# Kernel optimization log

Measured on AMD Instinct MI355X. Metric: run time of the kernel, lower is better.

The kernel has to match this reference:

```python
import jax, jax.numpy as jnp
import numpy as np

N = 8192        # total nodes in the batch of graphs
E = 262144      # edges (avg degree 32)
F_IN = 128      # input node features
G = 64          # graphs in batch
C = 10          # classes
K1, K2, K3 = 4096, 2048, 1024  # int(0.5*N), int(0.5*K1), int(0.5*K2)


def setup_inputs() -> dict:
    key = jax.random.key(0)
    ks = jax.random.split(key, 16)
    def lin(k, i, o):
        return jax.random.normal(k, (i, o), jnp.float32) / np.float32(np.sqrt(i))
    return {
        "x": jax.random.normal(ks[0], (N, F_IN), jnp.float32),
        "edge_index": jax.random.randint(ks[1], (2, E), 0, N),
        "batch": jnp.sort(jax.random.randint(ks[2], (N,), 0, G)),
        "W1": lin(ks[3], F_IN, 32), "b1": jnp.zeros((32,), jnp.float32),
        "W2": lin(ks[4], 32, 64),   "b2": jnp.zeros((64,), jnp.float32),
        "W3": lin(ks[5], 64, 128),  "b3": jnp.zeros((128,), jnp.float32),
        "W4": lin(ks[6], 128, 256), "b4": jnp.zeros((256,), jnp.float32),
        "W5": lin(ks[7], 384, 128), "b5": jnp.zeros((128,), jnp.float32),
        "W6": lin(ks[8], 192, 64),  "b6": jnp.zeros((64,), jnp.float32),
        "W7": lin(ks[9], 96, 32),   "b7": jnp.zeros((32,), jnp.float32),
        "p1": jax.random.normal(ks[10], (32,), jnp.float32),
        "p2": jax.random.normal(ks[11], (64,), jnp.float32),
        "p3": jax.random.normal(ks[12], (128,), jnp.float32),
        "Wl1": lin(ks[13], 64, 64),
        "Wc": lin(ks[14], 64, C), "bc": jnp.zeros((C,), jnp.float32),
    }


def _gcn(A, x, W, b):
    # PyG GCNConv (improved=False): out = D^-1/2 (A+I) D^-1/2 propagated src->dst.
    n = A.shape[0]
    Ah = A + jnp.eye(n, dtype=A.dtype)
    deg = Ah.sum(axis=0)                                  # degree at targets (cols)
    dinv = jnp.where(deg > 0, deg ** -0.5, 0.0).astype(A.dtype)
    An = dinv[:, None] * Ah * dinv[None, :]               # edge norm d[src]^-.5 * d[dst]^-.5
    return An.T @ (x @ W) + b                             # out[dst] += norm * (xW)[src]


def _gpool(A, x, p, k):
    # GPool: scores = Linear(x)/||p||, top-k select, gate by sigmoid, reindex dense adj.
    scores = (x @ p) / jnp.linalg.norm(p)                 # [n]
    vals, idx = jax.lax.top_k(scores, k)
    xp = x[idx] * jax.nn.sigmoid(vals)[:, None]
    Ap = (A[idx][:, idx] > 0).astype(x.dtype)             # dense_to_sparse rebinarizes
    return xp, Ap, idx


def reference(x, edge_index, batch, W1, b1, W2, b2, W3, b3, W4, b4, W5, b5,
              W6, b6, W7, b7, p1, p2, p3, Wl1, Wc, bc):
    elu = jax.nn.elu
    # to_dense_adj: dense N x N adjacency (duplicate edges accumulate)
    A = jnp.zeros((N, N), x.dtype).at[edge_index[0], edge_index[1]].add(1.0)
    x1 = elu(_gcn(A, x, W1, b1))
    x2, A2, i2 = _gpool(A, x1, p1, K1); x2 = elu(x2)
    x3 = elu(_gcn(A2, x2, W2, b2))
    x4, A4, i4 = _gpool(A2, x3, p2, K2); x4 = elu(x4)
    x5 = elu(_gcn(A4, x4, W3, b3))
    x6, A6, i6 = _gpool(A4, x5, p3, K3); x6 = elu(x6)
    x7 = elu(_gcn(A6, x6, W4, b4))
    u = jnp.zeros((K2, x7.shape[1]), x7.dtype).at[i6].set(x7)   # GUnpool
    x8 = elu(jnp.concatenate([u, x5], axis=1))
    x9 = elu(_gcn(A4, x8, W5, b5))
    u = jnp.zeros((K1, x9.shape[1]), x9.dtype).at[i4].set(x9)
    x10 = elu(jnp.concatenate([u, x3], axis=1))
    x11 = elu(_gcn(A2, x10, W6, b6))
    u = jnp.zeros((N, x11.shape[1]), x11.dtype).at[i2].set(x11)
    x12 = elu(jnp.concatenate([u, x1], axis=1))
    x13 = elu(_gcn(A, x12, W7, b7))
    gmax = jax.ops.segment_max(x13, batch, num_segments=G)      # global max pool
    gsum = jax.ops.segment_sum(x13, batch, num_segments=G)
    cnt = jax.ops.segment_sum(jnp.ones((N, 1), x13.dtype), batch, num_segments=G)
    h = elu(jnp.concatenate([gmax, gsum / cnt], axis=1))        # [G, 64]
    h = elu(h @ Wl1)
    return jax.nn.log_softmax(h @ Wc + bc, axis=-1)
```

## Files before the change

### kernel.cpp

```cpp
#include <hip/hip_runtime.h>
#include <math.h>

#define NN 8192
#define EE 262144
#define GG 64
#define CC 10
#define KK1 4096
#define KK2 2048
#define KK3 1024
#define PITCH 128

typedef unsigned long long ull;

__device__ __forceinline__ float eluf(float x) { return x > 0.f ? x : expm1f(x); }
__device__ __forceinline__ float sigf(float x) { return 1.f / (1.f + expf(-x)); }
__device__ __forceinline__ unsigned f2s(float f) {
    unsigned u = __float_as_uint(f);
    return (u & 0x80000000u) ? ~u : (u | 0x80000000u);
}

__global__ void k_init(const int* __restrict__ ei, unsigned* __restrict__ bitmap,
                       int* __restrict__ cnt1, int* __restrict__ csr1,
                       const int* __restrict__ batch, int* __restrict__ gstart,
                       const float* __restrict__ X, const float* __restrict__ W,
                       float* __restrict__ Y) {
    __shared__ float Xs[32][33];
    __shared__ float Ws[32][36];
    int tid = threadIdx.x;
    if ((int)blockIdx.x >= 1024) {
        int txn = tid & 7, tym = tid >> 3;
        int m0 = ((int)blockIdx.x - 1024) * 32;
        float4 acc = make_float4(0.f, 0.f, 0.f, 0.f);
        for (int k0 = 0; k0 < 128; k0 += 32) {
            int r = tid >> 3, c4 = (tid & 7) << 2;
            *(float4*)&Xs[r][c4] = *(const float4*)&X[(size_t)(m0 + r) * 128 + k0 + c4];
            *(float4*)&Ws[r][c4] = *(const float4*)&W[(size_t)(k0 + r) * 32 + c4];
            __syncthreads();
#pragma unroll 8
            for (int kk = 0; kk < 32; kk++) {
                float4 wv = *(const float4*)&Ws[kk][txn * 4];
                float xv = Xs[tym][kk];
                acc.x += xv * wv.x; acc.y += xv * wv.y;
                acc.z += xv * wv.z; acc.w += xv * wv.w;
            }
            __syncthreads();
        }
        *(float4*)&Y[(size_t)(m0 + tym) * 32 + txn * 4] = acc;
        return;
    }
    int e = blockIdx.x * 256 + tid;
    int s = ei[e], d = ei[EE + e];
    unsigned key = ((unsigned)s << 13) | (unsigned)d;
    unsigned old = atomicOr(&bitmap[key >> 5], 1u << (key & 31u));
    int dup = (old >> (key & 31u)) & 1;
    int pos = atomicAdd(&cnt1[d], 1);
    csr1[(d << 7) + pos] = dup ? (s | 0x80000000) : s;
    if (e < NN) {
        int g = batch[e];
        int prev = (e == 0) ? -1 : batch[e - 1];
        for (int gg = prev + 1; gg <= g; gg++) gstart[gg] = e;
        if (e == NN - 1)
            for (int gg = g + 1; gg <= GG; gg++) gstart[gg] = NN;
    }
}

template<int L1>
__global__ void k_pool_sub(const float* __restrict__ x, const float* __restrict__ score,
                           const int* __restrict__ idx, int k, int F,
                           float* __restrict__ xout, int nPool,
                           const int* __restrict__ csrP, const int* __restrict__ roffP,
                           const int* __restrict__ degP,
                           const int* __restrict__ invmap,
                           int* __restrict__ csrO, int* __restrict__ roffO,
                           int* __restrict__ degO, float* __restrict__ dinvO) {
    if ((int)blockIdx.x < nPool) {
        int t = blockIdx.x * 256 + threadIdx.x;
        if (t >= k * F) return;
        int r = t / F, f = t - r * F;
        int j = idx[r];
        xout[t] = eluf(x[(size_t)j * F + f] * sigf(score[j]));
        return;
    }
    int wid = (((int)blockIdx.x - nPool) * 256 + (int)threadIdx.x) >> 6;
    int lane = threadIdx.x & 63;
    if (wid >= k) return;
    int j = idx[wid];
    int j0 = L1 ? (j << 7) : roffP[j];
    int len = degP[j];
    int cnt = 0;
    for (int base = 0; base < len; base += 64) {
        bool sel = false;
        int val = 0;
        if (base + lane < len) {
            int e = csrP[j0 + base + lane];
            if (!L1 || e >= 0) {
                int s = L1 ? (e & 0x7fffffff) : e;
                int v = invmap[s];
                if (v > 0) { sel = true; val = v - 1; }
            }
        }
        ull m = __ballot(sel);
        if (sel) {
            int off = __popcll(m & ((1ull << lane) - 1ull));
            csrO[j0 + cnt + off] = val;
        }
        cnt += __popcll(m);
    }
    if (lane == 0) {
        roffO[wid] = j0;
        degO[wid] = cnt;
        dinvO[wid] = 1.f / sqrtf((float)(cnt + 1));
    }
}

__global__ void k_gemm(const float* __restrict__ X, const float* __restrict__ W,
                       float* __restrict__ Y, int M, int K, int F) {
    __shared__ float Xs[32][33];
    __shared__ float Ws[32][36];
    int tid = threadIdx.x;
    int txn = tid & 7, tym = tid >> 3;
    int m0 = blockIdx.x * 32, n0 = blockIdx.y * 32;
    float4 acc = make_float4(0.f, 0.f, 0.f, 0.f);
    for (int k0 = 0; k0 < K; k0 += 32) {
        {
            int r = tid >> 3, c4 = (tid & 7) << 2;
            *(float4*)&Xs[r][c4] = *(const float4*)&X[(size_t)(m0 + r) * K + k0 + c4];
            *(float4*)&Ws[r][c4] = *(const float4*)&W[(size_t)(k0 + r) * F + n0 + c4];
        }
        __syncthreads();
#pragma unroll 8
        for (int kk = 0; kk < 32; kk++) {
            float4 wv = *(const float4*)&Ws[kk][txn * 4];
            float xv = Xs[tym][kk];
            acc.x += xv * wv.x; acc.y += xv * wv.y;
            acc.z += xv * wv.z; acc.w += xv * wv.w;
        }
        __syncthreads();
    }
    *(float4*)&Y[(size_t)(m0 + tym) * F + n0 + txn * 4] = acc;
}

__global__ void k_gemm_up(const float* __restrict__ xl, const int* __restrict__ inv,
                          const float* __restrict__ xr, int Fl, int Fr,
                          const float* __restrict__ W, float* __restrict__ Y,
                          int M, int K, int F) {
    __shared__ float Xs[32][33];
    __shared__ float Ws[32][36];
    __shared__ int sIdx[32];
    int tid = threadIdx.x;
    int txn = tid & 7, tym = tid >> 3;
    int m0 = blockIdx.x * 32, n0 = blockIdx.y * 32;
    if (tid < 32) sIdx[tid] = inv[m0 + tid];
    float4 acc = make_float4(0.f, 0.f, 0.f, 0.f);
    __syncthreads();
    for (int k0 = 0; k0 < K; k0 += 32) {
        {
            int r = tid >> 3, c4 = (tid & 7) << 2;
            int kk = k0 + c4;
            float4 v;
            if (kk < Fl) {
                int rr = sIdx[r];
                v = (rr > 0) ? *(const float4*)&xl[(size_t)(rr - 1) * Fl + kk]
                             : make_float4(0.f, 0.f, 0.f, 0.f);
            } else {
                v = *(const float4*)&xr[(size_t)(m0 + r) * Fr + (kk - Fl)];
            }
            v.x = eluf(v.x); v.y = eluf(v.y); v.z = eluf(v.z); v.w = eluf(v.w);
            *(float4*)&Xs[r][c4] = v;
            *(float4*)&Ws[r][c4] = *(const float4*)&W[(size_t)(k0 + r) * F + n0 + c4];
        }
        __syncthreads();
#pragma unroll 8
        for (int kk = 0; kk < 32; kk++) {
            float4 wv = *(const float4*)&Ws[kk][txn * 4];
            float xv = Xs[tym][kk];
            acc.x += xv * wv.x; acc.y += xv * wv.y;
            acc.z += xv * wv.z; acc.w += xv * wv.w;
        }
        __syncthreads();
    }
    *(float4*)&Y[(size_t)(m0 + tym) * F + n0 + txn * 4] = acc;
}

template<int LOGF, int SCORE, int L1, int LS>
__global__ void k_prop(const int* __restrict__ csr, const int* __restrict__ roff,
                       const int* __restrict__ deg, const float* __restrict__ dinv,
                       const float* __restrict__ xW, const float* __restrict__ b,
                       float* __restrict__ xout, const float* __restrict__ p,
                       float* __restrict__ score) {
    constexpr int FQ = 1 << (LOGF - 2);
    constexpr int S = 1 << LS;
    constexpr int RL = FQ * S;
    const float4* xW4 = (const float4*)xW;
    int t = blockIdx.x * 256 + threadIdx.x;
    int d = t >> (LOGF - 2 + LS);
    int rem = t & (RL - 1);
    int q = rem >> LS, h = rem & (S - 1);
    int j0 = L1 ? (d << 7) : roff[d];
    int dg = deg[d];
    int j1 = j0 + dg;
    float dd = L1 ? (1.f / sqrtf((float)(dg + 1))) : dinv[d];
    int idx = (d << (LOGF - 2)) + q;
    float4 sum;
    if (h == 0) {
        float4 v0 = xW4[idx];
        sum = make_float4(dd * v0.x, dd * v0.y, dd * v0.z, dd * v0.w);
    } else {
        sum = make_float4(0.f, 0.f, 0.f, 0.f);
    }
    for (int j = j0 + h; j < j1; j += S) {
        int e = csr[j];
        int s = L1 ? (e & 0x7fffffff) : e;
        float ds = L1 ? (1.f / sqrtf((float)(deg[s] + 1))) : dinv[s];
        float4 xv = xW4[(s << (LOGF - 2)) + q];
        sum.x += ds * xv.x; sum.y += ds * xv.y;
        sum.z += ds * xv.z; sum.w += ds * xv.w;
    }
#pragma unroll
    for (int m = 1; m < S; m <<= 1) {
        sum.x += __shfl_xor(sum.x, m, 64);
        sum.y += __shfl_xor(sum.y, m, 64);
        sum.z += __shfl_xor(sum.z, m, 64);
        sum.w += __shfl_xor(sum.w, m, 64);
    }
    float4 bv = *(const float4*)&b[q << 2];
    float4 o;
    o.x = eluf(dd * sum.x + bv.x);
    o.y = eluf(dd * sum.y + bv.y);
    o.z = eluf(dd * sum.z + bv.z);
    o.w = eluf(dd * sum.w + bv.w);
    if (h == 0) ((float4*)xout)[idx] = o;
    if (SCORE) {
        float4 pv = *(const float4*)&p[q << 2];
        float sc = 0.f, nr = 0.f;
        if (h == 0) {
            sc = o.x * pv.x + o.y * pv.y + o.z * pv.z + o.w * pv.w;
            nr = pv.x * pv.x + pv.y * pv.y + pv.z * pv.z + pv.w * pv.w;
        }
#pragma unroll
        for (int m = RL >> 1; m >= 1; m >>= 1) {
            sc += __shfl_xor(sc, m, 64);
            nr += __shfl_xor(nr, m, 64);
        }
        if (rem == 0) score[d] = sc / sqrtf(nr);
    }
}

__device__ __forceinline__ ull cex_shfl(ull v, int st, bool takeMax) {
    ull pv = __shfl_xor(v, st, 64);
    return takeMax ? (v > pv ? v : pv) : (v < pv ? v : pv);
}
__device__ __forceinline__ void cexr(ull& a, ull& b, bool desc) {
    if (desc ? (a < b) : (a > b)) { ull x = a; a = b; b = x; }
}

__global__ void k_wsort(const float* __restrict__ score, ull* __restrict__ keys,
                        int last, int k, int* __restrict__ out_idx,
                        int* __restrict__ invmap) {
    __shared__ ull sk[2048];
    int tid = threadIdx.x;
    int base = blockIdx.x << 11;
    int giA = base + tid, giB = giA + 1024;
    ull a = ((ull)f2s(score[giA]) << 32) | (unsigned)(~giA);
    ull b = ((ull)f2s(score[giB]) << 32) | (unsigned)(~giB);
    for (int sz = 2; sz <= 2048; sz <<= 1) {
        int st = sz >> 1;
        if (st >= 64) {
            sk[tid] = a; sk[tid + 1024] = b;
            __syncthreads();
            for (; st >= 64; st >>= 1) {
                int i = ((tid & ~(st - 1)) << 1) | (tid & (st - 1));
                int j = i | st;
                ull u = sk[i], v = sk[j];
                bool desc = (((base + i) & sz) == 0);
                if (desc ? (u < v) : (u > v)) { sk[i] = v; sk[j] = u; }
                __syncthreads();
            }
            a = sk[tid]; b = sk[tid + 1024];
        }
        for (; st >= 1; st >>= 1) {
            bool low = (tid & st) == 0;
            bool descA = ((giA & sz) == 0);
            bool descB = ((giB & sz) == 0);
            a = cex_shfl(a, st, descA == low);
            b = cex_shfl(b, st, descB == low);
        }
    }
    if (last) {
        if (giA < k) {
            int j = (int)(~(unsigned)(a & 0xFFFFFFFFu));
            out_idx[giA] = j; invmap[j] = giA + 1;
        }
        if (giB < k) {
            int j = (int)(~(unsigned)(b & 0xFFFFFFFFu));
            out_idx[giB] = j; invmap[j] = giB + 1;
        }
    } else {
        keys[giA] = a; keys[giB] = b;
    }
}

__global__ void k_stage4k_m(ull* __restrict__ keys) {
    __shared__ ull sk[4096];
    int tid = threadIdx.x;
    int base = blockIdx.x << 12;
    bool desc = ((base & 4096) == 0);
    ull k0 = keys[base + tid], k1 = keys[base + tid + 1024];
    ull k2 = keys[base + tid + 2048], k3 = keys[base + tid + 3072];
    cexr(k0, k2, desc); cexr(k1, k3, desc);
    sk[tid] = k0; sk[tid + 1024] = k1; sk[tid + 2048] = k2; sk[tid + 3072] = k3;
    __syncthreads();
    for (int st = 1024; st >= 64; st >>= 1) {
        for (int pp = tid; pp < 2048; pp += 1024) {
            int i = ((pp & ~(st - 1)) << 1) | (pp & (st - 1));
            int j = i | st;
            ull u = sk[i], v = sk[j];
            if (desc ? (u < v) : (u > v)) { sk[i] = v; sk[j] = u; }
        }
        __syncthreads();
    }
    k0 = sk[tid]; k1 = sk[tid + 1024]; k2 = sk[tid + 2048]; k3 = sk[tid + 3072];
    for (int st = 32; st >= 1; st >>= 1) {
        bool low = (tid & st) == 0;
        k0 = cex_shfl(k0, st, desc == low);
        k1 = cex_shfl(k1, st, desc == low);
        k2 = cex_shfl(k2, st, desc == low);
        k3 = cex_shfl(k3, st, desc == low);
    }
    keys[base + tid] = k0; keys[base + tid + 1024] = k1;
    keys[base + tid + 2048] = k2; keys[base + tid + 3072] = k3;
}

__global__ void k_stage8k_f(const ull* __restrict__ keys, int* __restrict__ out_idx,
                            int* __restrict__ invmap) {
    __shared__ ull sk[4096];
    int tid = threadIdx.x;
    ull a0 = keys[tid],        a1 = keys[tid + 1024];
    ull a2 = keys[tid + 2048], a3 = keys[tid + 3072];
    ull b0 = keys[tid + 4096], b1 = keys[tid + 5120];
    ull b2 = keys[tid + 6144], b3 = keys[tid + 7168];
    cexr(a0, b0, true); cexr(a1, b1, true);
    cexr(a2, b2, true); cexr(a3, b3, true);
    cexr(a0, a2, true); cexr(a1, a3, true);
    sk[tid] = a0; sk[tid + 1024] = a1; sk[tid + 2048] = a2; sk[tid + 3072] = a3;
    __syncthreads();
    for (int st = 1024; st >= 64; st >>= 1) {
        for (int pp = tid; pp < 2048; pp += 1024) {
            int i = ((pp & ~(st - 1)) << 1) | (pp & (st - 1));
            int j = i | st;
            ull u = sk[i], v = sk[j];
            if (u < v) { sk[i] = v; sk[j] = u; }
        }
        __syncthreads();
    }
    a0 = sk[tid]; a1 = sk[tid + 1024]; a2 = sk[tid + 2048]; a3 = sk[tid + 3072];
    for (int st = 32; st >= 1; st >>= 1) {
        bool low = (tid & st) == 0;
        a0 = cex_shfl(a0, st, low);
        a1 = cex_shfl(a1, st, low);
        a2 = cex_shfl(a2, st, low);
        a3 = cex_shfl(a3, st, low);
    }
    int p, j;
    p = tid;        j = (int)(~(unsigned)(a0 & 0xFFFFFFFFu)); out_idx[p] = j; invmap[j] = p + 1;
    p = tid + 1024; j = (int)(~(unsigned)(a1 & 0xFFFFFFFFu)); out_idx[p] = j; invmap[j] = p + 1;
    p = tid + 2048; j = (int)(~(unsigned)(a2 & 0xFFFFFFFFu)); out_idx[p] = j; invmap[j] = p + 1;
    p = tid + 3072; j = (int)(~(unsigned)(a3 & 0xFFFFFFFFu)); out_idx[p] = j; invmap[j] = p + 1;
}

__global__ void k_stage4k_f(const ull* __restrict__ keys, int* __restrict__ out_idx,
                            int* __restrict__ invmap) {
    __shared__ ull sk[2048];
    int tid = threadIdx.x;
    ull a0 = keys[tid],        a1 = keys[tid + 1024];
    ull a2 = keys[tid + 2048], a3 = keys[tid + 3072];
    cexr(a0, a2, true); cexr(a1, a3, true);
    sk[tid] = a0; sk[tid + 1024] = a1;
    __syncthreads();
    for (int st = 1024; st >= 64; st >>= 1) {
        int i = ((tid & ~(st - 1)) << 1) | (tid & (st - 1));
        int j = i | st;
        ull u = sk[i], v = sk[j];
        if (u < v) { sk[i] = v; sk[j] = u; }
        __syncthreads();
    }
    a0 = sk[tid]; a1 = sk[tid + 1024];
    for (int st = 32; st >= 1; st >>= 1) {
        bool low = (tid & st) == 0;
        a0 = cex_shfl(a0, st, low);
        a1 = cex_shfl(a1, st, low);
    }
    int p, j;
    p = tid;        j = (int)(~(unsigned)(a0 & 0xFFFFFFFFu)); out_idx[p] = j; invmap[j] = p + 1;
    p = tid + 1024; j = (int)(~(unsigned)(a1 & 0xFFFFFFFFu)); out_idx[p] = j; invmap[j] = p + 1;
}

__global__ void k_seg2(const float* __restrict__ x13, const int* __restrict__ gstart,
                       float* __restrict__ gmaxf, float* __restrict__ gsum,
                       int* __restrict__ gcnt) {
    __shared__ float sm[8][32], ss[8][32];
    int g = blockIdx.x;
    int j0 = gstart[g], j1 = gstart[g + 1];
    int t = threadIdx.x;
    int f = t & 31, r = t >> 5;
    float m = -INFINITY, s = 0.f;
    for (int j = j0 + r; j < j1; j += 8) {
        float v = x13[(j << 5) + f];
        m = fmaxf(m, v);
        s += v;
    }
    sm[r][f] = m; ss[r][f] = s;
    __syncthreads();
    if (t < 32) {
        float mm = sm[0][t], sss = ss[0][t];
        for (int i = 1; i < 8; i++) { mm = fmaxf(mm, sm[i][t]); sss += ss[i][t]; }
        gmaxf[(g << 5) + t] = mm;
        gsum[(g << 5) + t] = sss;
        if (t == 0) gcnt[g] = j1 - j0;
    }
}

__global__ void k_head(const float* __restrict__ gmaxf, const float* __restrict__ gsum,
                       const int* __restrict__ gcnt, const float* __restrict__ Wl1,
                       const float* __restrict__ Wc, const float* __restrict__ bc,
                       float* __restrict__ out) {
    __shared__ float h0[GG * 64];
    __shared__ float h1[GG * 64];
    __shared__ float lg[GG * CC];
    int tid = threadIdx.x;
    for (int t = tid; t < GG * 64; t += blockDim.x) {
        int g = t >> 6, c = t & 63;
        float v;
        if (c < 32) v = gmaxf[(g << 5) + c];
        else v = gsum[(g << 5) + (c - 32)] / (float)gcnt[g];
        h0[t] = eluf(v);
    }
    __syncthreads();
    for (int t = tid; t < GG * 64; t += blockDim.x) {
        int g = t >> 6, j = t & 63;
        float s = 0.f;
        for (int k = 0; k < 64; k++) s += h0[(g << 6) + k] * Wl1[k * 64 + j];
        h1[t] = eluf(s);
    }
    __syncthreads();
    for (int t = tid; t < GG * CC; t += blockDim.x) {
        int g = t / CC, c = t - g * CC;
        float s = bc[c];
        for (int k = 0; k < 64; k++) s += h1[(g << 6) + k] * Wc[k * CC + c];
        lg[t] = s;
    }
    __syncthreads();
    if (tid < GG) {
        int g = tid;
        float m = -1e30f;
        for (int c = 0; c < CC; c++) m = fmaxf(m, lg[g * CC + c]);
        float se = 0.f;
        for (int c = 0; c < CC; c++) se += expf(lg[g * CC + c] - m);
        float lse = m + logf(se);
        for (int c = 0; c < CC; c++) out[g * CC + c] = lg[g * CC + c] - lse;
    }
}

static void run_topk(const float* score, ull* keys, int n, int k, int* out_idx,
                     int* invmap, hipStream_t stream) {
    if (n == 2048) {
        k_wsort<<<1, 1024, 0, stream>>>(score, keys, 1, k, out_idx, invmap);
    } else if (n == 4096) {
        k_wsort<<<2, 1024, 0, stream>>>(score, keys, 0, k, out_idx, invmap);
        k_stage4k_f<<<1, 1024, 0, stream>>>(keys, out_idx, invmap);
    } else {
        k_wsort<<<4, 1024, 0, stream>>>(score, keys, 0, k, out_idx, invmap);
        k_stage4k_m<<<2, 1024, 0, stream>>>(keys);
        k_stage8k_f<<<1, 1024, 0, stream>>>(keys, out_idx, invmap);
    }
}

extern "C" void kernel_launch(void* const* d_in, const int* in_sizes, int n_in,
                              void* d_out, int out_size, void* d_ws, size_t ws_size,
                              hipStream_t stream) {
    const float* x = (const float*)d_in[0];
    const int* ei = (const int*)d_in[1];
    const int* batch = (const int*)d_in[2];
    const float* W1 = (const float*)d_in[3];  const float* b1 = (const float*)d_in[4];
    const float* W2 = (const float*)d_in[5];  const float* b2 = (const float*)d_in[6];
    const float* W3 = (const float*)d_in[7];  const float* b3 = (const float*)d_in[8];
    const float* W4 = (const float*)d_in[9];  const float* b4 = (const float*)d_in[10];
    const float* W5 = (const float*)d_in[11]; const float* b5 = (const float*)d_in[12];
    const float* W6 = (const float*)d_in[13]; const float* b6 = (const float*)d_in[14];
    const float* W7 = (const float*)d_in[15]; const float* b7 = (const float*)d_in[16];
    const float* p1 = (const float*)d_in[17];
    const float* p2 = (const float*)d_in[18];
    const float* p3 = (const float*)d_in[19];
    const float* Wl1 = (const float*)d_in[20];
    const float* Wc = (const float*)d_in[21];
    const float* bc = (const float*)d_in[22];
    float* out = (float*)d_out;
    (void)in_sizes; (void)n_in; (void)out_size; (void)ws_size;

    char* w = (char*)d_ws;
    size_t off = 0;
    auto alloc = [&](size_t bytes) -> char* {
        char* p = w + off;
        off = (off + bytes + 255) & ~(size_t)255;
        return p;
    };

    size_t zero_begin = off;
    unsigned* bitmap = (unsigned*)alloc((size_t)NN * NN / 8);
    int* cnt1 = (int*)alloc(NN * 4);
    int* pos2 = (int*)alloc(NN * 4);
    int* inv4 = (int*)alloc(KK1 * 4);
    int* inv6 = (int*)alloc(KK2 * 4);
    size_t zero_len = off - zero_begin;

    float* dinv2 = (float*)alloc(KK1 * 4);
    float* dinv3 = (float*)alloc(KK2 * 4);
    float* dinv4 = (float*)alloc(KK3 * 4);
    int* roff2 = (int*)alloc(KK1 * 4); int* deg2 = (int*)alloc(KK1 * 4);
    int* roff3 = (int*)alloc(KK2 * 4); int* deg3 = (int*)alloc(KK2 * 4);
    int* roff4 = (int*)alloc(KK3 * 4); int* deg4 = (int*)alloc(KK3 * 4);
    int* csr1 = (int*)alloc((size_t)NN * PITCH * 4);
    int* csr2 = (int*)alloc((size_t)NN * PITCH * 4);
    int* csr3 = (int*)alloc((size_t)NN * PITCH * 4);
    int* csr4 = (int*)alloc((size_t)NN * PITCH * 4);
    float* xW = (float*)alloc((size_t)262144 * 4);
    float* x1 = (float*)alloc((size_t)NN * 32 * 4);
    float* x2 = (float*)alloc((size_t)KK1 * 32 * 4);
    float* x3 = (float*)alloc((size_t)KK1 * 64 * 4);
    float* x4 = (float*)alloc((size_t)KK2 * 64 * 4);
    float* x5 = (float*)alloc((size_t)KK2 * 128 * 4);
    float* x6 = (float*)alloc((size_t)KK3 * 128 * 4);
    float* x7 = (float*)alloc((size_t)KK3 * 256 * 4);
    float* x9 = (float*)alloc((size_t)KK2 * 128 * 4);
    float* x11 = (float*)alloc((size_t)KK1 * 64 * 4);
    float* x13 = (float*)alloc((size_t)NN * 32 * 4);
    float* score1 = (float*)alloc(NN * 4);
    float* score2 = (float*)alloc(KK1 * 4);
    float* score3 = (float*)alloc(KK2 * 4);
    int* i2 = (int*)alloc(KK1 * 4);
    int* i4 = (int*)alloc(KK2 * 4);
    int* i6 = (int*)alloc(KK3 * 4);
    ull* keys = (ull*)alloc((size_t)NN * 8);
    int* gstart = (int*)alloc((GG + 1) * 4);
    float* gmaxf = (float*)alloc(GG * 32 * 4);
    float* gsum = (float*)alloc(GG * 32 * 4);
    int* gcnt = (int*)alloc(GG * 4);

    hipMemsetAsync(w + zero_begin, 0, zero_len, stream);

    const int B = 256;
    k_init<<<1280, B, 0, stream>>>(ei, bitmap, cnt1, csr1, batch, gstart, x, W1, xW);

    k_prop<5, 1, 1, 3><<<2048, B, 0, stream>>>(csr1, nullptr, cnt1, nullptr, xW, b1,
                                               x1, p1, score1);

    run_topk(score1, keys, NN, KK1, i2, pos2, stream);
    k_pool_sub<1><<<512 + KK1 / 4, B, 0, stream>>>(x1, score1, i2, KK1, 32, x2, 512,
                                                   csr1, nullptr, cnt1, pos2,
                                                   csr2, roff2, deg2, dinv2);

    k_gemm<<<dim3(KK1 / 32, 2), B, 0, stream>>>(x2, W2, xW, KK1, 32, 64);
    k_prop<6, 1, 0, 2><<<1024, B, 0, stream>>>(csr2, roff2, deg2, dinv2, xW, b2,
                                               x3, p2, score2);

    run_topk(score2, keys, KK1, KK2, i4, inv4, stream);
    k_pool_sub<0><<<512 + KK2 / 4, B, 0, stream>>>(x3, score2, i4, KK2, 64, x4, 512,
                                                   csr2, roff2, deg2, inv4,
                                                   csr3, roff3, deg3, dinv3);

    k_gemm<<<dim3(KK2 / 32, 4), B, 0, stream>>>(x4, W3, xW, KK2, 64, 128);
    k_prop<7, 1, 0, 1><<<512, B, 0, stream>>>(csr3, roff3, deg3, dinv3, xW, b3,
                                              x5, p3, score3);

    run_topk(score3, keys, KK2, KK3, i6, inv6, stream);
    k_pool_sub<0><<<512 + KK3 / 4, B, 0, stream>>>(x5, score3, i6, KK3, 128, x6, 512,
                                                   csr3, roff3, deg3, inv6,
                                                   csr4, roff4, deg4, dinv4);

    k_gemm<<<dim3(KK3 / 32, 8), B, 0, stream>>>(x6, W4, xW, KK3, 128, 256);
    k_prop<8, 0, 0, 1><<<512, B, 0, stream>>>(csr4, roff4, deg4, dinv4, xW, b4,
                                              x7, nullptr, nullptr);

    k_gemm_up<<<dim3(KK2 / 32, 4), B, 0, stream>>>(x7, inv6, x5, 256, 128,
                                                   W5, xW, KK2, 384, 128);
    k_prop<7, 0, 0, 2><<<1024, B, 0, stream>>>(csr3, roff3, deg3, dinv3, xW, b5,
                                               x9, nullptr, nullptr);

    k_gemm_up<<<dim3(KK1 / 32, 2), B, 0, stream>>>(x9, inv4, x3, 128, 64,
                                                   W6, xW, KK1, 192, 64);
    k_prop<6, 0, 0, 2><<<1024, B, 0, stream>>>(csr2, roff2, deg2, dinv2, xW, b6,
                                               x11, nullptr, nullptr);

    k_gemm_up<<<dim3(NN / 32, 1), B, 0, stream>>>(x11, pos2, x1, 64, 32,
                                                  W7, xW, NN, 96, 32);
    k_prop<5, 0, 1, 3><<<2048, B, 0, stream>>>(csr1, nullptr, cnt1, nullptr, xW, b7,
                                               x13, nullptr, nullptr);

    k_seg2<<<GG, B, 0, stream>>>(x13, gstart, gmaxf, gsum, gcnt);
    k_head<<<1, 1024, 0, stream>>>(gmaxf, gsum, gcnt, Wl1, Wc, bc, out);
}
```

Before: 333.4 us.

## Replace bitmap edge dedup with warp-level dedup and fuse sort and head kernels

Drops the N×N/8-byte duplicate-edge bitmap. That removes its large memset and the random atomicOr traffic in k_init. Duplicate neighbours are now found inside the level-1 pool subgraph kernel by shuffle-comparing each row's up to 128 entries within a warp. The 4096-element top-k sort now runs as one full bitonic sort kernel (k_sort4k) instead of wsort plus a merge stage, and segment pooling is fused with the MLP head into one per-graph kernel. This saves launches and memory traffic, at the cost of an O(degree) serial shuffle loop per selected node and redundant per-block head computation.

```diff
diff --git a/kernel.cpp b/kernel.cpp
--- a/kernel.cpp
+++ b/kernel.cpp
@@ -19,11 +19,10 @@
     return (u & 0x80000000u) ? ~u : (u | 0x80000000u);
 }
 
-__global__ void k_init(const int* __restrict__ ei, unsigned* __restrict__ bitmap,
-                       int* __restrict__ cnt1, int* __restrict__ csr1,
-                       const int* __restrict__ batch, int* __restrict__ gstart,
-                       const float* __restrict__ X, const float* __restrict__ W,
-                       float* __restrict__ Y) {
+__global__ void k_init(const int* __restrict__ ei, int* __restrict__ cnt1,
+                       int* __restrict__ csr1, const int* __restrict__ batch,
+                       int* __restrict__ gstart, const float* __restrict__ X,
+                       const float* __restrict__ W, float* __restrict__ Y) {
     __shared__ float Xs[32][33];
     __shared__ float Ws[32][36];
     int tid = threadIdx.x;
@@ -50,11 +49,8 @@
     }
     int e = blockIdx.x * 256 + tid;
     int s = ei[e], d = ei[EE + e];
-    unsigned key = ((unsigned)s << 13) | (unsigned)d;
-    unsigned old = atomicOr(&bitmap[key >> 5], 1u << (key & 31u));
-    int dup = (old >> (key & 31u)) & 1;
     int pos = atomicAdd(&cnt1[d], 1);
-    csr1[(d << 7) + pos] = dup ? (s | 0x80000000) : s;
+    csr1[(d << 7) + pos] = s;
     if (e < NN) {
         int g = batch[e];
         int prev = (e == 0) ? -1 : batch[e - 1];
@@ -85,31 +81,59 @@
     int lane = threadIdx.x & 63;
     if (wid >= k) return;
     int j = idx[wid];
-    int j0 = L1 ? (j << 7) : roffP[j];
-    int len = degP[j];
     int cnt = 0;
-    for (int base = 0; base < len; base += 64) {
-        bool sel = false;
-        int val = 0;
-        if (base + lane < len) {
-            int e = csrP[j0 + base + lane];
-            if (!L1 || e >= 0) {
-                int s = L1 ? (e & 0x7fffffff) : e;
-                int v = invmap[s];
+    if (L1) {
+        int j0 = j << 7;
+        int len = degP[j];
+        int e0 = (lane < len) ? csrP[j0 + lane] : -1;
+        int e1 = (64 + lane < len) ? csrP[j0 + 64 + lane] : -1;
+        bool dup0 = false, dup1 = false;
+        for (int q = 0; q < len - 1; q++) {
+            int vq = (q < 64) ? __shfl(e0, q, 64) : __shfl(e1, q - 64, 64);
+            if (lane > q && e0 == vq) dup0 = true;
+            if (64 + lane > q && e1 == vq) dup1 = true;
+        }
+        {
+            bool sel = (lane < len) && !dup0;
+            int val = 0;
+            if (sel) { int v = invmap[e0]; if (v > 0) val = v - 1; else sel = false; }
+            ull m = __ballot(sel);
+            if (sel) { int off = __popcll(m & ((1ull << lane) - 1ull)); csrO[j0 + cnt + off] = val; }
+            cnt += __popcll(m);
+        }
+        {
+            bool sel = (64 + lane < len) && !dup1;
+            int val = 0;
+            if (sel) { int v = invmap[e1]; if (v > 0) val = v - 1; else sel = false; }
+            ull m = __ballot(sel);
+            if (sel) { int off = __popcll(m & ((1ull << lane) - 1ull)); csrO[j0 + cnt + off] = val; }
+            cnt += __popcll(m);
+        }
+        if (lane == 0) {
+            roffO[wid] = j0;
+            degO[wid] = cnt;
+            dinvO[wid] = 1.f / sqrtf((float)(cnt + 1));
+        }
+    } else {
+        int j0 = roffP[j];
+        int len = degP[j];
+        for (int base = 0; base < len; base += 64) {
+            bool sel = false;
+            int val = 0;
+            if (base + lane < len) {
+                int e = csrP[j0 + base + lane];
+                int v = invmap[e];
                 if (v > 0) { sel = true; val = v - 1; }
             }
-        }
-        ull m = __ballot(sel);
-        if (sel) {
-            int off = __popcll(m & ((1ull << lane) - 1ull));
-            csrO[j0 + cnt + off] = val;
-        }
-        cnt += __popcll(m);
-    }
-    if (lane == 0) {
-        roffO[wid] = j0;
-        degO[wid] = cnt;
-        dinvO[wid] = 1.f / sqrtf((float)(cnt + 1));
+            ull m = __ballot(sel);
+            if (sel) { int off = __popcll(m & ((1ull << lane) - 1ull)); csrO[j0 + cnt + off] = val; }
+            cnt += __popcll(m);
+        }
+        if (lane == 0) {
+            roffO[wid] = j0;
+            degO[wid] = cnt;
+            dinvO[wid] = 1.f / sqrtf((float)(cnt + 1));
+        }
     }
 }
 
@@ -209,8 +233,7 @@
         sum = make_float4(0.f, 0.f, 0.f, 0.f);
     }
     for (int j = j0 + h; j < j1; j += S) {
-        int e = csr[j];
-        int s = L1 ? (e & 0x7fffffff) : e;
+        int s = csr[j];
         float ds = L1 ? (1.f / sqrtf((float)(deg[s] + 1))) : dinv[s];
         float4 xv = xW4[(s << (LOGF - 2)) + q];
         sum.x += ds * xv.x; sum.y += ds * xv.y;
@@ -300,35 +323,51 @@
     }
 }
 
-__global__ void k_stage4k_m(ull* __restrict__ keys) {
+__global__ void k_sort4k(const float* __restrict__ score, ull* __restrict__ keys,
+                         int last, int k, int* __restrict__ out_idx,
+                         int* __restrict__ invmap) {
     __shared__ ull sk[4096];
     int tid = threadIdx.x;
     int base = blockIdx.x << 12;
-    bool desc = ((base & 4096) == 0);
-    ull k0 = keys[base + tid], k1 = keys[base + tid + 1024];
-    ull k2 = keys[base + tid + 2048], k3 = keys[base + tid + 3072];
-    cexr(k0, k2, desc); cexr(k1, k3, desc);
-    sk[tid] = k0; sk[tid + 1024] = k1; sk[tid + 2048] = k2; sk[tid + 3072] = k3;
-    __syncthreads();
-    for (int st = 1024; st >= 64; st >>= 1) {
-        for (int pp = tid; pp < 2048; pp += 1024) {
-            int i = ((pp & ~(st - 1)) << 1) | (pp & (st - 1));
-            int j = i | st;
-            ull u = sk[i], v = sk[j];
-            if (desc ? (u < v) : (u > v)) { sk[i] = v; sk[j] = u; }
-        }
-        __syncthreads();
-    }
-    k0 = sk[tid]; k1 = sk[tid + 1024]; k2 = sk[tid + 2048]; k3 = sk[tid + 3072];
-    for (int st = 32; st >= 1; st >>= 1) {
-        bool low = (tid & st) == 0;
-        k0 = cex_shfl(k0, st, desc == low);
-        k1 = cex_shfl(k1, st, desc == low);
-        k2 = cex_shfl(k2, st, desc == low);
-        k3 = cex_shfl(k3, st, desc == low);
-    }
-    keys[base + tid] = k0; keys[base + tid + 1024] = k1;
-    keys[base + tid + 2048] = k2; keys[base + tid + 3072] = k3;
+    int p0 = base + tid, p1 = p0 + 1024, p2 = p0 + 2048, p3 = p0 + 3072;
+    ull k0 = ((ull)f2s(score[p0]) << 32) | (unsigned)(~p0);
+    ull k1 = ((ull)f2s(score[p1]) << 32) | (unsigned)(~p1);
+    ull k2 = ((ull)f2s(score[p2]) << 32) | (unsigned)(~p2);
+    ull k3 = ((ull)f2s(score[p3]) << 32) | (unsigned)(~p3);
+    for (int sz = 2; sz <= 4096; sz <<= 1) {
+        int st = sz >> 1;
+        if (st >= 64) {
+            sk[tid] = k0; sk[tid + 1024] = k1; sk[tid + 2048] = k2; sk[tid + 3072] = k3;
+            __syncthreads();
+            for (; st >= 64; st >>= 1) {
+                for (int pp = tid; pp < 2048; pp += 1024) {
+                    int i = ((pp & ~(st - 1)) << 1) | (pp & (st - 1));
+                    int jj = i | st;
+                    ull u = sk[i], v = sk[jj];
+                    bool desc = (((base + i) & sz) == 0);
+                    if (desc ? (u < v) : (u > v)) { sk[i] = v; sk[jj] = u; }
+                }
+                __syncthreads();
+            }
+            k0 = sk[tid]; k1 = sk[tid + 1024]; k2 = sk[tid + 2048]; k3 = sk[tid + 3072];
+        }
+        for (; st >= 1; st >>= 1) {
+            bool low = (tid & st) == 0;
+            k0 = cex_shfl(k0, st, ((p0 & sz) == 0) == low);
+            k1 = cex_shfl(k1, st, ((p1 & sz) == 0) == low);
+            k2 = cex_shfl(k2, st, ((p2 & sz) == 0) == low);
+            k3 = cex_shfl(k3, st, ((p3 & sz) == 0) == low);
+        }
+    }
+    if (last) {
+        int j;
+        if (p0 < k) { j = (int)(~(unsigned)(k0 & 0xFFFFFFFFu)); out_idx[p0] = j; invmap[j] = p0 + 1; }
+        if (p1 < k) { j = (int)(~(unsigned)(k1 & 0xFFFFFFFFu)); out_idx[p1] = j; invmap[j] = p1 + 1; }
+        if (p2 < k) { j = (int)(~(unsigned)(k2 & 0xFFFFFFFFu)); out_idx[p2] = j; invmap[j] = p2 + 1; }
+        if (p3 < k) { j = (int)(~(unsigned)(k3 & 0xFFFFFFFFu)); out_idx[p3] = j; invmap[j] = p3 + 1; }
+    } else {
+        keys[p0] = k0; keys[p1] = k1; keys[p2] = k2; keys[p3] = k3;
+    }
 }
 
 __global__ void k_stage8k_f(const ull* __restrict__ keys, int* __restrict__ out_idx,
@@ -368,37 +407,11 @@
     p = tid + 3072; j = (int)(~(unsigned)(a3 & 0xFFFFFFFFu)); out_idx[p] = j; invmap[j] = p + 1;
 }
 
-__global__ void k_stage4k_f(const ull* __restrict__ keys, int* __restrict__ out_idx,
-                            int* __restrict__ invmap) {
-    __shared__ ull sk[2048];
-    int tid = threadIdx.x;
-    ull a0 = keys[tid],        a1 = keys[tid + 1024];
-    ull a2 = keys[tid + 2048], a3 = keys[tid + 3072];
-    cexr(a0, a2, true); cexr(a1, a3, true);
-    sk[tid] = a0; sk[tid + 1024] = a1;
-    __syncthreads();
-    for (int st = 1024; st >= 64; st >>= 1) {
-        int i = ((tid & ~(st - 1)) << 1) | (tid & (st - 1));
-        int j = i | st;
-        ull u = sk[i], v = sk[j];
-        if (u < v) { sk[i] = v; sk[j] = u; }
-        __syncthreads();
-    }
-    a0 = sk[tid]; a1 = sk[tid + 1024];
-    for (int st = 32; st >= 1; st >>= 1) {
-        bool low = (tid & st) == 0;
-        a0 = cex_shfl(a0, st, low);
-        a1 = cex_shfl(a1, st, low);
-    }
-    int p, j;
-    p = tid;        j = (int)(~(unsigned)(a0 & 0xFFFFFFFFu)); out_idx[p] = j; invmap[j] = p + 1;
-    p = tid + 1024; j = (int)(~(unsigned)(a1 & 0xFFFFFFFFu)); out_idx[p] = j; invmap[j] = p + 1;
-}
-
-__global__ void k_seg2(const float* __restrict__ x13, const int* __restrict__ gstart,
-                       float* __restrict__ gmaxf, float* __restrict__ gsum,
-                       int* __restrict__ gcnt) {
+__global__ void k_finale(const float* __restrict__ x13, const int* __restrict__ gstart,
+                         const float* __restrict__ Wl1, const float* __restrict__ Wc,
+                         const float* __restrict__ bc, float* __restrict__ out) {
     __shared__ float sm[8][32], ss[8][32];
+    __shared__ float h0[64], h1[64], lg[CC];
     int g = blockIdx.x;
     int j0 = gstart[g], j1 = gstart[g + 1];
     int t = threadIdx.x;
@@ -414,50 +427,29 @@
     if (t < 32) {
         float mm = sm[0][t], sss = ss[0][t];
         for (int i = 1; i < 8; i++) { mm = fmaxf(mm, sm[i][t]); sss += ss[i][t]; }
-        gmaxf[(g << 5) + t] = mm;
-        gsum[(g << 5) + t] = sss;
-        if (t == 0) gcnt[g] = j1 - j0;
-    }
-}
-
-__global__ void k_head(const float* __restrict__ gmaxf, const float* __restrict__ gsum,
-                       const int* __restrict__ gcnt, const float* __restrict__ Wl1,
-                       const float* __restrict__ Wc, const float* __restrict__ bc,
-                       float* __restrict__ out) {
-    __shared__ float h0[GG * 64];
-    __shared__ float h1[GG * 64];
-    __shared__ float lg[GG * CC];
-    int tid = threadIdx.x;
-    for (int t = tid; t < GG * 64; t += blockDim.x) {
-        int g = t >> 6, c = t & 63;
-        float v;
-        if (c < 32) v = gmaxf[(g << 5) + c];
-        else v = gsum[(g << 5) + (c - 32)] / (float)gcnt[g];
-        h0[t] = eluf(v);
+        h0[t] = eluf(mm);
+        h0[32 + t] = eluf(sss / (float)(j1 - j0));
     }
     __syncthreads();
-    for (int t = tid; t < GG * 64; t += blockDim.x) {
-        int g = t >> 6, j = t & 63;
-        float s = 0.f;
-        for (int k = 0; k < 64; k++) s += h0[(g << 6) + k] * Wl1[k * 64 + j];
-        h1[t] = eluf(s);
+    if (t < 64) {
+        float sum = 0.f;
+        for (int kk = 0; kk < 64; kk++) sum += h0[kk] * Wl1[kk * 64 + t];
+        h1[t] = eluf(sum);
     }
     __syncthreads();
-    for (int t = tid; t < GG * CC; t += blockDim.x) {
-        int g = t / CC, c = t - g * CC;
-        float s = bc[c];
-        for (int k = 0; k < 64; k++) s += h1[(g << 6) + k] * Wc[k * CC + c];
-        lg[t] = s;
+    if (t < CC) {
+        float sum = bc[t];
+        for (int kk = 0; kk < 64; kk++) sum += h1[kk] * Wc[kk * CC + t];
+        lg[t] = sum;
     }
     __syncthreads();
-    if (tid < GG) {
-        int g = tid;
-        float m = -1e30f;
-        for (int c = 0; c < CC; c++) m = fmaxf(m, lg[g * CC + c]);
+    if (t == 0) {
+        float mm = -1e30f;
+        for (int c = 0; c < CC; c++) mm = fmaxf(mm, lg[c]);
         float se = 0.f;
-        for (int c = 0; c < CC; c++) se += expf(lg[g * CC + c] - m);
-        float lse = m + logf(se);
-        for (int c = 0; c < CC; c++) out[g * CC + c] = lg[g * CC + c] - lse;
+        for (int c = 0; c < CC; c++) se += expf(lg[c] - mm);
+        float lse = mm + logf(se);
+        for (int c = 0; c < CC; c++) out[g * CC + c] = lg[c] - lse;
     }
 }
 
@@ -466,11 +458,9 @@
     if (n == 2048) {
         k_wsort<<<1, 1024, 0, stream>>>(score, keys, 1, k, out_idx, invmap);
     } else if (n == 4096) {
-        k_wsort<<<2, 1024, 0, stream>>>(score, keys, 0, k, out_idx, invmap);
-        k_stage4k_f<<<1, 1024, 0, stream>>>(keys, out_idx, invmap);
+        k_sort4k<<<1, 1024, 0, stream>>>(score, keys, 1, k, out_idx, invmap);
     } else {
-        k_wsort<<<4, 1024, 0, stream>>>(score, keys, 0, k, out_idx, invmap);
-        k_stage4k_m<<<2, 1024, 0, stream>>>(keys);
+        k_sort4k<<<2, 1024, 0, stream>>>(score, keys, 0, k, out_idx, invmap);
         k_stage8k_f<<<1, 1024, 0, stream>>>(keys, out_idx, invmap);
     }
 }
@@ -506,7 +496,6 @@
     };
 
     size_t zero_begin = off;
-    unsigned* bitmap = (unsigned*)alloc((size_t)NN * NN / 8);
     int* cnt1 = (int*)alloc(NN * 4);
     int* pos2 = (int*)alloc(NN * 4);
     int* inv4 = (int*)alloc(KK1 * 4);
@@ -542,14 +531,11 @@
     int* i6 = (int*)alloc(KK3 * 4);
     ull* keys = (ull*)alloc((size_t)NN * 8);
     int* gstart = (int*)alloc((GG + 1) * 4);
-    float* gmaxf = (float*)alloc(GG * 32 * 4);
-    float* gsum = (float*)alloc(GG * 32 * 4);
-    int* gcnt = (int*)alloc(GG * 4);
 
     hipMemsetAsync(w + zero_begin, 0, zero_len, stream);
 
     const int B = 256;
-    k_init<<<1280, B, 0, stream>>>(ei, bitmap, cnt1, csr1, batch, gstart, x, W1, xW);
+    k_init<<<1280, B, 0, stream>>>(ei, cnt1, csr1, batch, gstart, x, W1, xW);
 
     k_prop<5, 1, 1, 3><<<2048, B, 0, stream>>>(csr1, nullptr, cnt1, nullptr, xW, b1,
                                                x1, p1, score1);
@@ -596,6 +582,5 @@
     k_prop<5, 0, 1, 3><<<2048, B, 0, stream>>>(csr1, nullptr, cnt1, nullptr, xW, b7,
                                                x13, nullptr, nullptr);
 
-    k_seg2<<<GG, B, 0, stream>>>(x13, gstart, gmaxf, gsum, gcnt);
-    k_head<<<1, 1024, 0, stream>>>(gmaxf, gsum, gcnt, Wl1, Wc, bc, out);
-}
+    k_finale<<<GG, B, 0, stream>>>(x13, gstart, Wl1, Wc, bc, out);
+}
```

Result: slower. 341.6 us (+2.5%).
